# Performance work log

Measured on AMD Instinct MI355X. Metric: run time of the kernel, lower is better.

The kernel has to match this reference:

```python
import jax, jax.numpy as jnp
import numpy as np
from jax import lax

K = 3      # kernel_size
PAD = 1    # padding
OG = 2     # offset groups


def _conv2d(x, w, b):
    y = lax.conv_general_dilated(x, w, (1, 1), [(PAD, PAD), (PAD, PAD)],
                                 dimension_numbers=('NCHW', 'OIHW', 'NCHW'))
    return y + b[None, :, None, None]


def _deform_conv2d(x, offset, mask, weight):
    # torchvision-style modulated deform_conv2d (v2), stride=1, dilation=1,
    # zero out-of-bounds, offset layout [B, OG*K*K*2, H, W] with (dy, dx) pairs.
    B, C, H, W = x.shape
    O = weight.shape[0]
    K2 = K * K
    Cg = C // OG

    ki, kj = jnp.meshgrid(jnp.arange(K), jnp.arange(K), indexing='ij')
    ki = ki.reshape(K2)
    kj = kj.reshape(K2)
    base_y = jnp.arange(H)[None, :] - PAD + ki[:, None]   # [K2, H]
    base_x = jnp.arange(W)[None, :] - PAD + kj[:, None]   # [K2, W]

    off = offset.reshape(B, OG, K2, 2, H, W)
    py = off[:, :, :, 0] + base_y[None, None, :, :, None].astype(x.dtype)  # [B,OG,K2,H,W]
    px = off[:, :, :, 1] + base_x[None, None, :, None, :].astype(x.dtype)
    m = mask.reshape(B, OG, K2, H, W)

    y0f = jnp.floor(py)
    x0f = jnp.floor(px)
    wy1 = py - y0f   # bilinear weights, grads flow through py/px
    wx1 = px - x0f
    y0 = y0f.astype(jnp.int32)
    x0 = x0f.astype(jnp.int32)
    y1 = y0 + 1
    x1 = x0 + 1

    img = x.reshape(B, OG, Cg, H * W)

    def gather(yi, xi):
        valid = (yi >= 0) & (yi < H) & (xi >= 0) & (xi < W)
        idx = jnp.clip(yi, 0, H - 1) * W + jnp.clip(xi, 0, W - 1)          # [B,OG,K2,H,W]
        v = jnp.take_along_axis(img[:, :, :, None, :],
                                idx.reshape(B, OG, 1, K2, H * W), axis=-1)
        return v.reshape(B, OG, Cg, K2, H, W) * valid[:, :, None].astype(x.dtype)

    v00 = gather(y0, x0)
    v01 = gather(y0, x1)
    v10 = gather(y1, x0)
    v11 = gather(y1, x1)

    wy1e = wy1[:, :, None]   # [B,OG,1,K2,H,W]
    wx1e = wx1[:, :, None]
    val = (v00 * (1 - wy1e) * (1 - wx1e)
           + v01 * (1 - wy1e) * wx1e
           + v10 * wy1e * (1 - wx1e)
           + v11 * wy1e * wx1e)
    val = val * m[:, :, None]                               # modulation mask

    wr = weight.reshape(O, OG, Cg, K2)
    return jnp.einsum('ogck,bgckhw->bohw', wr, val)


def setup_inputs() -> dict:
    key = jax.random.key(0)
    k1, k2, k3, k4, k5 = jax.random.split(key, 5)
    B, C, O, H, W = 4, 64, 64, 128, 128
    K2 = K * K
    x = jax.random.normal(k1, (B, C, H, W), dtype=jnp.float32)
    w_main = jax.random.normal(k2, (O, C, K, K), dtype=jnp.float32) / np.sqrt(C * K2)
    w_off = jax.random.normal(k3, (2 * OG * K2, C, K, K), dtype=jnp.float32) * 0.01
    b_off = jax.random.normal(k4, (2 * OG * K2,), dtype=jnp.float32) * 0.01
    w_mask = jnp.full((OG * K2, C, K, K), 0.5, dtype=jnp.float32)  # init_mask = 0.5
    b_mask = jax.random.normal(k5, (OG * K2,), dtype=jnp.float32) * 0.01
    return {"x": x, "w_main": w_main, "w_off": w_off, "b_off": b_off,
            "w_mask": w_mask, "b_mask": b_mask}


def reference(x, w_main, w_off, b_off, w_mask, b_mask):
    offset = _conv2d(x, w_off, b_off)
    mask = jax.nn.sigmoid(_conv2d(x, w_mask, b_mask))
    return _deform_conv2d(x, offset, mask, w_main)
```

## Files before the change

### kernel.cpp

```cpp
#include <hip/hip_runtime.h>
#include <math.h>

#define BB 4
#define C 64
#define O 64
#define H 128
#define W 128
#define K2 9
#define HW (H*W)
#define NOFF 36
#define NMSK 18

typedef __bf16 bf16;
typedef bf16 bf16x8 __attribute__((ext_vector_type(8)));
typedef float f32x4 __attribute__((ext_vector_type(4)));
typedef unsigned short u16x4 __attribute__((ext_vector_type(4)));

#define BSTR 60
#define VAL_BYTES 20480
#define SMEM_BYTES 35840
#define NW_TOTAL 73728
#define WFRAG 18432

__device__ inline unsigned short f2h_bits(float f) {
  _Float16 h = (_Float16)f;
  return __builtin_bit_cast(unsigned short, h);
}
__device__ inline float h2f(unsigned short u) {
  return (float)__builtin_bit_cast(_Float16, u);
}

__global__ __launch_bounds__(256) void prep_all(
    const float* __restrict__ x, const float* __restrict__ w_main,
    const float* __restrict__ w_off, const float* __restrict__ w_mask,
    unsigned short* __restrict__ xT16, bf16* __restrict__ wfC,
    bf16* __restrict__ wfM) {
  __shared__ float tile[64][65];
  int tid = threadIdx.x;
  int b = blockIdx.x >> 8;
  int p0 = (blockIdx.x & 255) * 64;
#pragma unroll
  for (int it = 0; it < 16; ++it) {
    int c = it * 4 + (tid >> 6);
    tile[c][tid & 63] = x[(size_t)(b * C + c) * HW + p0 + (tid & 63)];
  }
  __syncthreads();
#pragma unroll
  for (int it = 0; it < 4; ++it) {
    int p = it * 16 + (tid >> 4);
    int cq = tid & 15;
    u16x4 o;
#pragma unroll
    for (int j = 0; j < 4; ++j) {
      bf16 t = (bf16)tile[cq * 4 + j][p];
      o[j] = __builtin_bit_cast(unsigned short, t);
    }
    *(u16x4*)&xT16[(size_t)(b * HW + p0 + p) * C + cq * 4] = o;
  }
  int i = blockIdx.x * 256 + tid;
  if (i < NW_TOTAL) {
    int which = (i >= 36864);
    int ii = which ? i - 36864 : i;
    int j = ii & 7;
    int l = (ii >> 3) & 63;
    int rest = ii >> 9;
    int to = rest & 3;
    int kk = (rest >> 2) % 9;
    int ph = (rest >> 2) / 9;
    int m = to * 16 + (l & 15);
    int u = kk * 32 + (l >> 4) * 8 + j;
    int tap = u >> 5;
    int c1 = u & 31;
    if (!which) {
      int c = ph * 32 + c1;
      float v = (m < NOFF) ? w_off[(m * C + c) * K2 + tap]
                : (m < 54) ? w_mask[((m - NOFF) * C + c) * K2 + tap]
                           : 0.f;
      wfC[ii] = (bf16)v;
    } else {
      wfM[ii] = (bf16)w_main[(m * C + ph * 32 + c1) * K2 + tap];
    }
  }
}

template <int KK0, int NKK>
__device__ inline void mfma_chunk(const bf16* __restrict__ wb,
                                  const bf16* __restrict__ val, int row,
                                  int q4, int lane, f32x4* acc) {
#pragma unroll
  for (int t = 0; t < NKK; ++t) {
    int kk = KK0 + t;
    bf16x8 bfr = *(const bf16x8*)(val + ((t * 64 + row) * 32 + q4 * 8));
#pragma unroll
    for (int to = 0; to < 4; ++to) {
      bf16x8 afr = *(const bf16x8*)(wb + (size_t)((kk * 4 + to) * 64 + lane) * 8);
      acc[to] = __builtin_amdgcn_mfma_f32_16x16x32_bf16(afr, bfr, acc[to], 0, 0, 0);
    }
  }
}

__global__ __launch_bounds__(256, 4) void fused_deform(
    const bf16* __restrict__ xT, const bf16* __restrict__ wfC,
    const bf16* __restrict__ wfM, const float* __restrict__ b_off,
    const float* __restrict__ b_mask, float* __restrict__ out) {
  __shared__ __align__(16) char smem[SMEM_BYTES];
  bf16* val = (bf16*)smem;
  unsigned int (*buf)[BSTR] = (unsigned int (*)[BSTR])(smem + VAL_BYTES);
  float* bufF = (float*)(smem + VAL_BYTES);
  bf16x8* stage16 = (bf16x8*)(smem + VAL_BYTES);
  float* valF = (float*)smem;

  const int tid = threadIdx.x;
  const int lane = tid & 63;
  const int wv = tid >> 6;
  const int n16 = lane & 15;
  const int q4 = lane >> 4;
  const int chunk = tid & 3;
  const int pg = tid >> 2;
  const int row = wv * 16 + n16;

  const int b = blockIdx.x >> 8;
  const int ti = blockIdx.x & 255;
  const int h0 = ti >> 1;
  const int w0 = (ti & 1) * 64;
  const bf16* xb = xT + (size_t)b * HW * C;

  bf16x8 zero8;
#pragma unroll
  for (int j = 0; j < 8; ++j) zero8[j] = (bf16)0.f;

  f32x4 accC[4] = {{0.f,0.f,0.f,0.f},{0.f,0.f,0.f,0.f},
                   {0.f,0.f,0.f,0.f},{0.f,0.f,0.f,0.f}};
#pragma unroll 1
  for (int ph = 0; ph < 2; ++ph) {
    if (ph) __syncthreads();
#pragma unroll
    for (int it = 0; it < 4; ++it) {
      int id = it * 256 + tid;
      if (id < 816) {
        int q2 = id & 3;
        int wp = (id >> 2) % 68;
        int r = (id >> 2) / 68;
        int yy = h0 + r - 1;
        int xx = w0 + wp - 1;
        bf16x8 v = zero8;
        if ((unsigned)yy < (unsigned)H && (unsigned)xx < (unsigned)W)
          v = *(const bf16x8*)(xb + (size_t)((yy << 7) + xx) * C + ph * 32 + q2 * 8);
        stage16[id] = v;
      }
    }
    __syncthreads();
#pragma unroll
    for (int t = 0; t < 5; ++t) {
      int tap = t;
      bf16x8 v = stage16[((tap / 3) * 68 + pg + tap % 3) * 4 + chunk];
      *(bf16x8*)(val + ((t * 64 + pg) * 32 + chunk * 8)) = v;
    }
    __syncthreads();
    mfma_chunk<0, 5>(wfC + (size_t)ph * WFRAG, val, row, q4, lane, accC);
    __syncthreads();
#pragma unroll
    for (int t = 0; t < 4; ++t) {
      int tap = 5 + t;
      bf16x8 v = stage16[((tap / 3) * 68 + pg + tap % 3) * 4 + chunk];
      *(bf16x8*)(val + ((t * 64 + pg) * 32 + chunk * 8)) = v;
    }
    __syncthreads();
    mfma_chunk<5, 4>(wfC + (size_t)ph * WFRAG, val, row, q4, lane, accC);
  }
  {
#pragma unroll
    for (int to = 0; to < 4; ++to)
#pragma unroll
      for (int r = 0; r < 4; ++r) {
        int o = to * 16 + q4 * 4 + r;
        float a = accC[to][r];
        if (o < NOFF) {
          bufF[row * BSTR + o] = a + b_off[o];
        } else if (o < 54) {
          float s = a + b_mask[o - NOFF];
          bufF[row * BSTR + o] = 1.f / (1.f + __expf(-s));
        }
      }
  }
  __syncthreads();

  unsigned int rW0[5], rW1[5], rCo[5];
#pragma unroll
  for (int it = 0; it < 5; ++it) {
    int t = it * 256 + tid;
    if (t < 1152) {
      int p = t & 63;
      int gk = t >> 6;
      int g = gk / 9, tap = gk % 9;
      float offy = bufF[p * BSTR + 2 * gk];
      float offx = bufF[p * BSTR + 2 * gk + 1];
      float m = bufF[p * BSTR + NOFF + gk];
      float py = offy + (float)(h0 + tap / 3 - 1);
      float px = offx + (float)(w0 + p + tap % 3 - 1);
      float y0f = floorf(py), x0f = floorf(px);
      float wy1 = py - y0f, wx1 = px - x0f;
      float wy0 = 1.f - wy1, wx0 = 1.f - wx1;
      int y0 = (int)y0f, x0 = (int)x0f;
      int y1 = y0 + 1, x1 = x0 + 1;
      bool y0ok = (unsigned)y0 < (unsigned)H, y1ok = (unsigned)y1 < (unsigned)H;
      bool x0ok = (unsigned)x0 < (unsigned)W, x1ok = (unsigned)x1 < (unsigned)W;
      float w00 = (y0ok && x0ok) ? wy0 * wx0 * m : 0.f;
      float w01 = (y0ok && x1ok) ? wy0 * wx1 * m : 0.f;
      float w10 = (y1ok && x0ok) ? wy1 * wx0 * m : 0.f;
      float w11 = (y1ok && x1ok) ? wy1 * wx1 * m : 0.f;
      unsigned int y0c = (unsigned)min(max(y0, 0), H - 1);
      unsigned int y1c = (unsigned)min(max(y1, 0), H - 1);
      unsigned int x0c = (unsigned)min(max(x0, 0), W - 1);
      unsigned int x1c = (unsigned)min(max(x1, 0), W - 1);
      rW0[it] = (unsigned)f2h_bits(w00) | ((unsigned)f2h_bits(w01) << 16);
      rW1[it] = (unsigned)f2h_bits(w10) | ((unsigned)f2h_bits(w11) << 16);
      rCo[it] = y0c | (x0c << 8) | (y1c << 16) | (x1c << 24);
    }
  }
  __syncthreads();
#pragma unroll
  for (int it = 0; it < 5; ++it) {
    int t = it * 256 + tid;
    if (t < 1152) {
      int p = t & 63;
      int gk = t >> 6;
      buf[p][2 * gk] = rW0[it];
      buf[p][2 * gk + 1] = rW1[it];
      buf[p][NOFF + gk] = rCo[it];
    }
  }
  __syncthreads();

  f32x4 accM[4] = {{0.f,0.f,0.f,0.f},{0.f,0.f,0.f,0.f},
                   {0.f,0.f,0.f,0.f},{0.f,0.f,0.f,0.f}};
#pragma unroll 1
  for (int g = 0; g < 2; ++g) {
    if (g) __syncthreads();
    const bf16* bb = xb + g * 32 + chunk * 8;
#pragma unroll 1
    for (int kc = 0; kc < 2; ++kc) {
      int tap0 = kc ? 5 : 0;
      int ntap = kc ? 4 : 5;
      if (kc) __syncthreads();
#pragma unroll 5
      for (int t = 0; t < ntap; ++t) {
        int tap = tap0 + t;
        int gk = g * 9 + tap;
        unsigned int wab = buf[pg][2 * gk];
        unsigned int wcd = buf[pg][2 * gk + 1];
        unsigned int pk = buf[pg][NOFF + gk];
        float w00 = h2f(wab & 0xffff), w01 = h2f(wab >> 16);
        float w10 = h2f(wcd & 0xffff), w11 = h2f(wcd >> 16);
        int r0 = (int)(pk & 255) << 7;
        int x0 = (int)((pk >> 8) & 255);
        int r1 = (int)((pk >> 16) & 255) << 7;
        int x1 = (int)(pk >> 24);
        bf16x8 v00 = *(const bf16x8*)(bb + (size_t)(r0 + x0) * C);
        bf16x8 v01 = *(const bf16x8*)(bb + (size_t)(r0 + x1) * C);
        bf16x8 v10 = *(const bf16x8*)(bb + (size_t)(r1 + x0) * C);
        bf16x8 v11 = *(const bf16x8*)(bb + (size_t)(r1 + x1) * C);
        bf16x8 res;
#pragma unroll
        for (int j = 0; j < 8; ++j) {
          float v = (float)v00[j] * w00 + (float)v01[j] * w01 +
                    (float)v10[j] * w10 + (float)v11[j] * w11;
          res[j] = (bf16)v;
        }
        *(bf16x8*)(val + ((t * 64 + pg) * 32 + chunk * 8)) = res;
      }
      __syncthreads();
      if (kc)
        mfma_chunk<5, 4>(wfM + (size_t)g * WFRAG, val, row, q4, lane, accM);
      else
        mfma_chunk<0, 5>(wfM + (size_t)g * WFRAG, val, row, q4, lane, accM);
    }
  }

  __syncthreads();
  {
#pragma unroll
    for (int to = 0; to < 4; ++to)
#pragma unroll
      for (int r = 0; r < 4; ++r)
        valF[(to * 16 + q4 * 4 + r) * 68 + row] = accM[to][r];
  }
  __syncthreads();
  {
    float* ob = out + (size_t)b * O * HW + (h0 << 7) + w0;
#pragma unroll
    for (int it = 0; it < 4; ++it) {
      int id = it * 256 + tid;
      int o = id >> 4, seg = id & 15;
      f32x4 v = *(f32x4*)&valF[o * 68 + seg * 4];
      *(f32x4*)&ob[(size_t)o * HW + seg * 4] = v;
    }
  }
}

extern "C" void kernel_launch(void* const* d_in, const int* in_sizes, int n_in,
                              void* d_out, int out_size, void* d_ws,
                              size_t ws_size, hipStream_t stream) {
  const float* x = (const float*)d_in[0];
  const float* w_main = (const float*)d_in[1];
  const float* w_off = (const float*)d_in[2];
  const float* b_off = (const float*)d_in[3];
  const float* w_mask = (const float*)d_in[4];
  const float* b_mask = (const float*)d_in[5];
  float* out = (float*)d_out;

  unsigned short* xT16 = (unsigned short*)d_ws;
  bf16* wfC = (bf16*)(xT16 + (size_t)BB * HW * C);
  bf16* wfM = wfC + 36864;

  prep_all<<<1024, 256, 0, stream>>>(x, w_main, w_off, w_mask, xT16, wfC, wfM);
  fused_deform<<<1024, 256, 0, stream>>>((const bf16*)xT16, wfC, wfM, b_off,
                                         b_mask, out);
}
```

Before: 123.5 us.

## Merge prep and deform kernels into one launch with grid barrier

Fuses the transpose/weight-prep kernel and the deform kernel into a single launch separated by an atomic-counter grid-wide barrier, removing a kernel boundary. It also cuts shared memory (smaller value tile, tighter buffer stride) and raises the occupancy hint to 6 blocks per CU so all 1024 blocks can be co-resident. MFMA chunking is reworked to 3 taps per chunk, with each wave owning one output-channel tile and iterating over pixel tiles. The grid barrier relies on every block being resident at once, so it risks deadlock or spin overhead, and it adds a memset launch.

Result: slower. 214.1 us (+73.4%).

```diff
diff --git a/kernel.cpp b/kernel.cpp
--- a/kernel.cpp
+++ b/kernel.cpp
@@ -9,18 +9,19 @@
 #define K2 9
 #define HW (H*W)
 #define NOFF 36
-#define NMSK 18
 
 typedef __bf16 bf16;
 typedef bf16 bf16x8 __attribute__((ext_vector_type(8)));
 typedef float f32x4 __attribute__((ext_vector_type(4)));
-typedef unsigned short u16x4 __attribute__((ext_vector_type(4)));
-
-#define BSTR 60
-#define VAL_BYTES 20480
-#define SMEM_BYTES 35840
+typedef unsigned short u16x8 __attribute__((ext_vector_type(8)));
+
+#define BSTR 57
+#define VAL_BYTES 12288
+#define BUF_BYTES (64*BSTR*4)
+#define SMEM_BYTES (VAL_BYTES + BUF_BYTES)
+#define WFRAG 18432
 #define NW_TOTAL 73728
-#define WFRAG 18432
+#define NBLK 1024
 
 __device__ inline unsigned short f2h_bits(float f) {
   _Float16 h = (_Float16)f;
@@ -30,35 +31,59 @@
   return (float)__builtin_bit_cast(_Float16, u);
 }
 
-__global__ __launch_bounds__(256) void prep_all(
+__device__ inline void mfma3(const bf16* __restrict__ wb, int kk0,
+                             const bf16* __restrict__ val, int wv, int n16,
+                             int q4, int lane, f32x4* acc) {
+#pragma unroll
+  for (int t = 0; t < 3; ++t) {
+    int kk = kk0 + t;
+    bf16x8 afr = *(const bf16x8*)(wb + (size_t)((kk * 4 + wv) * 64 + lane) * 8);
+#pragma unroll
+    for (int qq = 0; qq < 4; ++qq) {
+      bf16x8 bfr = *(const bf16x8*)(val + ((t * 64 + qq * 16 + n16) * 32 + q4 * 8));
+      acc[qq] = __builtin_amdgcn_mfma_f32_16x16x32_bf16(afr, bfr, acc[qq], 0, 0, 0);
+    }
+  }
+}
+
+__global__ __launch_bounds__(256, 6) void mega(
     const float* __restrict__ x, const float* __restrict__ w_main,
     const float* __restrict__ w_off, const float* __restrict__ w_mask,
-    unsigned short* __restrict__ xT16, bf16* __restrict__ wfC,
-    bf16* __restrict__ wfM) {
-  __shared__ float tile[64][65];
-  int tid = threadIdx.x;
-  int b = blockIdx.x >> 8;
-  int p0 = (blockIdx.x & 255) * 64;
-#pragma unroll
-  for (int it = 0; it < 16; ++it) {
-    int c = it * 4 + (tid >> 6);
-    tile[c][tid & 63] = x[(size_t)(b * C + c) * HW + p0 + (tid & 63)];
-  }
-  __syncthreads();
-#pragma unroll
-  for (int it = 0; it < 4; ++it) {
-    int p = it * 16 + (tid >> 4);
-    int cq = tid & 15;
-    u16x4 o;
-#pragma unroll
-    for (int j = 0; j < 4; ++j) {
-      bf16 t = (bf16)tile[cq * 4 + j][p];
-      o[j] = __builtin_bit_cast(unsigned short, t);
-    }
-    *(u16x4*)&xT16[(size_t)(b * HW + p0 + p) * C + cq * 4] = o;
-  }
-  int i = blockIdx.x * 256 + tid;
-  if (i < NW_TOTAL) {
+    const float* __restrict__ b_off, const float* __restrict__ b_mask,
+    unsigned short* xT16, bf16* wfC, bf16* wfM, float* __restrict__ out,
+    unsigned int* bar) {
+  __shared__ __align__(16) char smem[SMEM_BYTES];
+  const int tid = threadIdx.x;
+  const int b = blockIdx.x >> 8;
+  const int ti = blockIdx.x & 255;
+
+  {
+    float (*tile)[68] = (float (*)[68])smem;
+    int p0 = ti * 64;
+#pragma unroll
+    for (int it = 0; it < 4; ++it) {
+      int c = it * 16 + (tid >> 4);
+      int p4 = (tid & 15) * 4;
+      *(f32x4*)&tile[c][p4] =
+          *(const f32x4*)(x + (size_t)(b * C + c) * HW + p0 + p4);
+    }
+    __syncthreads();
+#pragma unroll
+    for (int it = 0; it < 2; ++it) {
+      int t = it * 256 + tid;
+      int p = t >> 3;
+      int h8 = t & 7;
+      u16x8 o;
+#pragma unroll
+      for (int j = 0; j < 8; ++j) {
+        bf16 v = (bf16)tile[h8 * 8 + j][p];
+        o[j] = __builtin_bit_cast(unsigned short, v);
+      }
+      *(u16x8*)&xT16[(size_t)(b * HW + p0 + p) * C + h8 * 8] = o;
+    }
+  }
+  if (tid < 72) {
+    int i = blockIdx.x * 72 + tid;
     int which = (i >= 36864);
     int ii = which ? i - 36864 : i;
     int j = ii & 7;
@@ -81,49 +106,33 @@
       wfM[ii] = (bf16)w_main[(m * C + ph * 32 + c1) * K2 + tap];
     }
   }
-}
-
-template <int KK0, int NKK>
-__device__ inline void mfma_chunk(const bf16* __restrict__ wb,
-                                  const bf16* __restrict__ val, int row,
-                                  int q4, int lane, f32x4* acc) {
-#pragma unroll
-  for (int t = 0; t < NKK; ++t) {
-    int kk = KK0 + t;
-    bf16x8 bfr = *(const bf16x8*)(val + ((t * 64 + row) * 32 + q4 * 8));
-#pragma unroll
-    for (int to = 0; to < 4; ++to) {
-      bf16x8 afr = *(const bf16x8*)(wb + (size_t)((kk * 4 + to) * 64 + lane) * 8);
-      acc[to] = __builtin_amdgcn_mfma_f32_16x16x32_bf16(afr, bfr, acc[to], 0, 0, 0);
-    }
-  }
-}
-
-__global__ __launch_bounds__(256, 4) void fused_deform(
-    const bf16* __restrict__ xT, const bf16* __restrict__ wfC,
-    const bf16* __restrict__ wfM, const float* __restrict__ b_off,
-    const float* __restrict__ b_mask, float* __restrict__ out) {
-  __shared__ __align__(16) char smem[SMEM_BYTES];
+
+  __syncthreads();
+  if (tid == 0) {
+    __threadfence();
+    __hip_atomic_fetch_add(bar, 1u, __ATOMIC_ACQ_REL, __HIP_MEMORY_SCOPE_AGENT);
+    while (__hip_atomic_load(bar, __ATOMIC_ACQUIRE, __HIP_MEMORY_SCOPE_AGENT) <
+           NBLK)
+      __builtin_amdgcn_s_sleep(32);
+    __threadfence();
+  }
+  __syncthreads();
+
   bf16* val = (bf16*)smem;
   unsigned int (*buf)[BSTR] = (unsigned int (*)[BSTR])(smem + VAL_BYTES);
   float* bufF = (float*)(smem + VAL_BYTES);
   bf16x8* stage16 = (bf16x8*)(smem + VAL_BYTES);
   float* valF = (float*)smem;
 
-  const int tid = threadIdx.x;
   const int lane = tid & 63;
   const int wv = tid >> 6;
   const int n16 = lane & 15;
   const int q4 = lane >> 4;
   const int chunk = tid & 3;
   const int pg = tid >> 2;
-  const int row = wv * 16 + n16;
-
-  const int b = blockIdx.x >> 8;
-  const int ti = blockIdx.x & 255;
   const int h0 = ti >> 1;
   const int w0 = (ti & 1) * 64;
-  const bf16* xb = xT + (size_t)b * HW * C;
+  const bf16* xb = (const bf16*)xT16 + (size_t)b * HW * C;
 
   bf16x8 zero8;
 #pragma unroll
@@ -133,7 +142,7 @@
                    {0.f,0.f,0.f,0.f},{0.f,0.f,0.f,0.f}};
 #pragma unroll 1
   for (int ph = 0; ph < 2; ++ph) {
-    if (ph) __syncthreads();
+    __syncthreads();
 #pragma unroll
     for (int it = 0; it < 4; ++it) {
       int id = it * 256 + tid;
@@ -150,38 +159,35 @@
       }
     }
     __syncthreads();
-#pragma unroll
-    for (int t = 0; t < 5; ++t) {
-      int tap = t;
-      bf16x8 v = stage16[((tap / 3) * 68 + pg + tap % 3) * 4 + chunk];
-      *(bf16x8*)(val + ((t * 64 + pg) * 32 + chunk * 8)) = v;
-    }
-    __syncthreads();
-    mfma_chunk<0, 5>(wfC + (size_t)ph * WFRAG, val, row, q4, lane, accC);
-    __syncthreads();
-#pragma unroll
-    for (int t = 0; t < 4; ++t) {
-      int tap = 5 + t;
-      bf16x8 v = stage16[((tap / 3) * 68 + pg + tap % 3) * 4 + chunk];
-      *(bf16x8*)(val + ((t * 64 + pg) * 32 + chunk * 8)) = v;
-    }
-    __syncthreads();
-    mfma_chunk<5, 4>(wfC + (size_t)ph * WFRAG, val, row, q4, lane, accC);
+#pragma unroll 1
+    for (int kc = 0; kc < 3; ++kc) {
+      if (kc) __syncthreads();
+#pragma unroll
+      for (int t = 0; t < 3; ++t) {
+        int tap = kc * 3 + t;
+        bf16x8 v = stage16[((tap / 3) * 68 + pg + tap % 3) * 4 + chunk];
+        *(bf16x8*)(val + ((t * 64 + pg) * 32 + chunk * 8)) = v;
+      }
+      __syncthreads();
+      mfma3(wfC + (size_t)ph * WFRAG, kc * 3, val, wv, n16, q4, lane, accC);
+    }
   }
   {
 #pragma unroll
-    for (int to = 0; to < 4; ++to)
+    for (int qq = 0; qq < 4; ++qq) {
+      int p = qq * 16 + n16;
 #pragma unroll
       for (int r = 0; r < 4; ++r) {
-        int o = to * 16 + q4 * 4 + r;
-        float a = accC[to][r];
+        int o = wv * 16 + q4 * 4 + r;
+        float a = accC[qq][r];
         if (o < NOFF) {
-          bufF[row * BSTR + o] = a + b_off[o];
+          bufF[p * BSTR + o] = a + b_off[o];
         } else if (o < 54) {
           float s = a + b_mask[o - NOFF];
-          bufF[row * BSTR + o] = 1.f / (1.f + __expf(-s));
+          bufF[p * BSTR + o] = 1.f / (1.f + __expf(-s));
         }
       }
+    }
   }
   __syncthreads();
 
@@ -236,16 +242,13 @@
                    {0.f,0.f,0.f,0.f},{0.f,0.f,0.f,0.f}};
 #pragma unroll 1
   for (int g = 0; g < 2; ++g) {
-    if (g) __syncthreads();
     const bf16* bb = xb + g * 32 + chunk * 8;
 #pragma unroll 1
-    for (int kc = 0; kc < 2; ++kc) {
-      int tap0 = kc ? 5 : 0;
-      int ntap = kc ? 4 : 5;
-      if (kc) __syncthreads();
-#pragma unroll 5
-      for (int t = 0; t < ntap; ++t) {
-        int tap = tap0 + t;
+    for (int kc = 0; kc < 3; ++kc) {
+      if (g || kc) __syncthreads();
+#pragma unroll
+      for (int t = 0; t < 3; ++t) {
+        int tap = kc * 3 + t;
         int gk = g * 9 + tap;
         unsigned int wab = buf[pg][2 * gk];
         unsigned int wcd = buf[pg][2 * gk + 1];
@@ -270,20 +273,19 @@
         *(bf16x8*)(val + ((t * 64 + pg) * 32 + chunk * 8)) = res;
       }
       __syncthreads();
-      if (kc)
-        mfma_chunk<5, 4>(wfM + (size_t)g * WFRAG, val, row, q4, lane, accM);
-      else
-        mfma_chunk<0, 5>(wfM + (size_t)g * WFRAG, val, row, q4, lane, accM);
+      mfma3(wfM + (size_t)g * WFRAG, kc * 3, val, wv, n16, q4, lane, accM);
     }
   }
 
   __syncthreads();
   {
 #pragma unroll
-    for (int to = 0; to < 4; ++to)
+    for (int qq = 0; qq < 4; ++qq) {
+      int p = qq * 16 + n16;
 #pragma unroll
       for (int r = 0; r < 4; ++r)
-        valF[(to * 16 + q4 * 4 + r) * 68 + row] = accM[to][r];
+        valF[(wv * 16 + q4 * 4 + r) * 68 + p] = accM[qq][r];
+    }
   }
   __syncthreads();
   {
@@ -312,8 +314,9 @@
   unsigned short* xT16 = (unsigned short*)d_ws;
   bf16* wfC = (bf16*)(xT16 + (size_t)BB * HW * C);
   bf16* wfM = wfC + 36864;
-
-  prep_all<<<1024, 256, 0, stream>>>(x, w_main, w_off, w_mask, xT16, wfC, wfM);
-  fused_deform<<<1024, 256, 0, stream>>>((const bf16*)xT16, wfC, wfM, b_off,
-                                         b_mask, out);
-}
+  unsigned int* bar = (unsigned int*)((char*)d_ws + 8536064);
+
+  hipMemsetAsync(bar, 0, 4, stream);
+  mega<<<NBLK, 256, 0, stream>>>(x, w_main, w_off, w_mask, b_off, b_mask,
+                                 xT16, wfC, wfM, out, bar);
+}
```
